# Optimization experiments

Measured on AMD Instinct MI355X. Metric: run time of the kernel, lower is better.

The kernel has to match this reference:

```python
import jax, jax.numpy as jnp
import numpy as np
from jax import lax

THD = 0.8  # Lowe ratio-test threshold (module init kwarg `thd`)


def setup_inputs() -> dict:
    key = jax.random.key(0)
    k1, k2 = jax.random.split(key)
    desc1 = jax.random.normal(k1, (16384, 128), dtype=jnp.float32)
    desc2 = jax.random.normal(k2, (16384, 128), dtype=jnp.float32)
    return {"desc1": desc1, "desc2": desc2}


def _cdist(a, b):
    # Euclidean pairwise distances, (B1, B2), same math as torch.cdist(p=2)
    sq_a = jnp.sum(a * a, axis=-1, keepdims=True)          # (B1, 1)
    sq_b = jnp.sum(b * b, axis=-1)                          # (B2,)
    d2 = sq_a + sq_b - 2.0 * (a @ b.T)                      # (B1, B2)
    return jnp.sqrt(jnp.maximum(d2, 0.0))


def reference(desc1, desc2):
    cost = _cdist(desc1, desc2)                             # (B1, B2)
    # two smallest distances per row
    neg_vals, idxs_in_2 = lax.top_k(-cost, 2)               # (B1, 2) each
    vals = -neg_vals
    ratio = vals[:, 0] / vals[:, 1]                         # (B1,)
    mask = ratio <= THD                                     # (B1,) bool
    # jit-compatible padded outputs: masked-out rows carry 0 distance; the
    # boolean mask selects the valid (idxs_in1, idxs_in2) match rows, which is
    # the compaction torch does with boolean indexing.
    match_dists = jnp.where(mask, ratio, 0.0)               # (B1,)
    idxs_in1 = jnp.arange(desc1.shape[0], dtype=jnp.int32)
    matches_idxs = jnp.stack([idxs_in1, idxs_in_2[:, 0].astype(jnp.int32)], axis=1)  # (B1, 2)
    return match_dists, matches_idxs, mask
```

## Files before the change

kernel.cpp:

```cpp
#include <hip/hip_runtime.h>
#include <math.h>
#include <float.h>
#include <stdint.h>


typedef __attribute__((ext_vector_type(4))) float     f32x4;
typedef __attribute__((ext_vector_type(8))) _Float16  half8;

#define D_     128
#define BM_    256
#define BN_    32
#define CS_    8
#define PARTS_ 8

__device__ __forceinline__ void gload_lds16(const void* g, void* l) {
  auto gp = (const __attribute__((address_space(1))) unsigned int*)(uintptr_t)g;
  auto lp = (__attribute__((address_space(3))) unsigned int*)(uintptr_t)l;
  __builtin_amdgcn_global_load_lds(gp, lp, 16, 0, 0);
}

__global__ void norms_kernel(const float* __restrict__ d1,
                             const float* __restrict__ d2,
                             float* __restrict__ sq, int B) {
  int gid  = blockIdx.x * blockDim.x + threadIdx.x;
  int wid  = gid >> 6;
  int lane = gid & 63;
  if (wid >= 2 * B) return;
  const float* src = (wid < B) ? (d1 + (size_t)wid * D_)
                               : (d2 + (size_t)(wid - B) * D_);
  float2 v = ((const float2*)src)[lane];
  float s = fmaf(v.x, v.x, v.y * v.y);
  #pragma unroll
  for (int off = 32; off > 0; off >>= 1) s += __shfl_down(s, off, 64);
  if (lane == 0) sq[wid] = s;
}

__global__ void convert_kernel(const float* __restrict__ d1, const float* __restrict__ d2,
                               _Float16* __restrict__ Ahi, _Float16* __restrict__ Alo,
                               _Float16* __restrict__ BhiP, _Float16* __restrict__ BloP,
                               int B) {
  int i = blockIdx.x * blockDim.x + threadIdx.x;
  int total = B * 16;
  if (i >= 2 * total) return;
  bool isB = i >= total;
  int j    = isB ? i - total : i;
  int desc = j >> 4;
  int seg  = j & 15;
  const float* src = (isB ? d2 : d1) + (size_t)desc * D_ + seg * 8;
  float4 v0 = *(const float4*)(src);
  float4 v1 = *(const float4*)(src + 4);
  half8 hv, lv;
  float e[8] = {v0.x, v0.y, v0.z, v0.w, v1.x, v1.y, v1.z, v1.w};
  #pragma unroll
  for (int q = 0; q < 8; ++q) {
    _Float16 h = (_Float16)e[q];
    _Float16 l = (_Float16)(e[q] - (float)h);
    if (isB) { h = (_Float16)(-2.0f) * h; l = (_Float16)(-2.0f) * l; }
    hv[q] = h; lv[q] = l;
  }
  if (!isB) {
    *(half8*)(Ahi + (size_t)desc * D_ + seg * 8) = hv;
    *(half8*)(Alo + (size_t)desc * D_ + seg * 8) = lv;
  } else {
    int t   = desc >> 5, cloc = desc & 31;
    int nf  = cloc >> 4, c15  = cloc & 15;
    int kk  = seg >> 2,  gq   = seg & 3;
    size_t off = (size_t)t * 4096 + kk * 1024 + nf * 512 + gq * 128 + c15 * 8;
    *(half8*)(BhiP + off) = hv;
    *(half8*)(BloP + off) = lv;
  }
}

__global__ __launch_bounds__(256, 2)
void nn_mfma(const _Float16* __restrict__ Ahi, const _Float16* __restrict__ Alo,
             const _Float16* __restrict__ BhiP, const _Float16* __restrict__ BloP,
             const float* __restrict__ sqb,
             float* __restrict__ p_d0, float* __restrict__ p_d1,
             int* __restrict__ p_j0, int B) {
  extern __shared__ char smem[];
  float* sq_lds = (float*)(smem + 49152);
  const int tid  = threadIdx.x;
  const int lane = tid & 63;
  const int wid  = tid >> 6;
  const int l15  = lane & 15;
  const int g    = lane >> 4;

  const int nrb   = B / BM_;
  const int rb    = blockIdx.x % nrb;
  const int cspl  = blockIdx.x / nrb;
  const int i0    = rb * BM_;
  const int niter = (B / CS_) / BN_;
  const int tile0 = cspl * niter;

  half8 ah[4][4], al[4][4];
  #pragma unroll
  for (int mf = 0; mf < 4; ++mf) {
    int row = i0 + wid * 64 + mf * 16 + l15;
    const _Float16* pa = Ahi + (size_t)row * D_ + g * 8;
    const _Float16* pl = Alo + (size_t)row * D_ + g * 8;
    #pragma unroll
    for (int kk = 0; kk < 4; ++kk) {
      ah[mf][kk] = *(const half8*)(pa + kk * 32);
      al[mf][kk] = *(const half8*)(pl + kk * 32);
    }
  }

  {
    const float* sqs = sqb + cspl * 2048;
    #pragma unroll
    for (int e = 0; e < 2; ++e) {
      int idx = tid + e * 256;
      float4 v = ((const float4*)sqs)[idx];
      ((float4*)sq_lds)[idx] = v;
    }
  }

  const _Float16* srcW = ((wid < 2) ? BhiP : BloP)
                       + (size_t)tile0 * 4096 + (wid & 1) * 2048 + lane * 8;
  char* ldsW = smem + (wid >> 1) * 8192 + (wid & 1) * 4096;
  auto stage = [&](int bufbase, int it) {
    const _Float16* s = srcW + (size_t)it * 4096;
    char* l = ldsW + bufbase;
    #pragma unroll
    for (int e = 0; e < 4; ++e) gload_lds16(s + e * 512, l + e * 1024);
  };

  float best0[16], best1[16]; int bj[16];
  #pragma unroll
  for (int s = 0; s < 16; ++s) { best0[s] = FLT_MAX; best1[s] = FLT_MAX; bj[s] = 0x7fffffff; }

  const int colg0 = tile0 * BN_ + l15;

  stage(0, 0);
  stage(16384, 1);
  asm volatile("s_waitcnt vmcnt(4)" ::: "memory");
  asm volatile("s_waitcnt lgkmcnt(0)" ::: "memory");
  __builtin_amdgcn_s_barrier();
  asm volatile("" ::: "memory");

  float sjc0 = sq_lds[l15];
  float sjc1 = sq_lds[16 + l15];

  int bcur = 0, bstage = 32768;
  for (int it = 0; it < niter; ++it) {
    if (it + 2 < niter) stage(bstage, it + 2);
    float sjn0 = 0.f, sjn1 = 0.f;
    if (it + 1 < niter) {
      sjn0 = sq_lds[(it + 1) * 32 + l15];
      sjn1 = sq_lds[(it + 1) * 32 + 16 + l15];
    }

    f32x4 acc[4][2];
    __builtin_amdgcn_s_setprio(1);
    #pragma unroll
    for (int kk = 0; kk < 4; ++kk) {
      half8 bh[2], bl[2];
      #pragma unroll
      for (int nf = 0; nf < 2; ++nf) {
        bh[nf] = *(const half8*)(smem + bcur + kk * 2048 + nf * 1024 + lane * 16);
        bl[nf] = *(const half8*)(smem + bcur + 8192 + kk * 2048 + nf * 1024 + lane * 16);
      }
      #pragma unroll
      for (int mf = 0; mf < 4; ++mf)
        #pragma unroll
        for (int nf = 0; nf < 2; ++nf) {
          if (kk == 0) {
            float sj = nf ? sjc1 : sjc0;
            f32x4 c0 = {sj, sj, sj, sj};
            acc[mf][nf] = __builtin_amdgcn_mfma_f32_16x16x32_f16(ah[mf][0], bh[nf], c0, 0, 0, 0);
          } else {
            acc[mf][nf] = __builtin_amdgcn_mfma_f32_16x16x32_f16(ah[mf][kk], bh[nf], acc[mf][nf], 0, 0, 0);
          }
        }
      #pragma unroll
      for (int mf = 0; mf < 4; ++mf)
        #pragma unroll
        for (int nf = 0; nf < 2; ++nf)
          acc[mf][nf] = __builtin_amdgcn_mfma_f32_16x16x32_f16(ah[mf][kk], bl[nf], acc[mf][nf], 0, 0, 0);
      #pragma unroll
      for (int mf = 0; mf < 4; ++mf)
        #pragma unroll
        for (int nf = 0; nf < 2; ++nf)
          acc[mf][nf] = __builtin_amdgcn_mfma_f32_16x16x32_f16(al[mf][kk], bh[nf], acc[mf][nf], 0, 0, 0);
    }
    __builtin_amdgcn_s_setprio(0);

    #pragma unroll
    for (int nf = 0; nf < 2; ++nf) {
      int colg = colg0 + it * BN_ + nf * 16;
      #pragma unroll
      for (int mf = 0; mf < 4; ++mf)
        #pragma unroll
        for (int r = 0; r < 4; ++r) {
          int s = mf * 4 + r;
          float t = acc[mf][nf][r];
          best1[s] = __builtin_amdgcn_fmed3f(t, best0[s], best1[s]);
          bool lt0 = t < best0[s];
          best0[s] = fminf(t, best0[s]);
          bj[s]    = lt0 ? colg : bj[s];
        }
    }

    if (it + 2 < niter) asm volatile("s_waitcnt vmcnt(4)" ::: "memory");
    else                asm volatile("s_waitcnt vmcnt(0)" ::: "memory");
    __builtin_amdgcn_s_barrier();
    asm volatile("" ::: "memory");

    sjc0 = sjn0; sjc1 = sjn1;
    bcur   = (bcur   == 32768) ? 0 : bcur   + 16384;
    bstage = (bstage == 32768) ? 0 : bstage + 16384;
  }

  #pragma unroll
  for (int off = 1; off < 16; off <<= 1) {
    #pragma unroll
    for (int s = 0; s < 16; ++s) {
      float e0 = __shfl_xor(best0[s], off, 64);
      float e1 = __shfl_xor(best1[s], off, 64);
      int   f0 = __shfl_xor(bj[s],    off, 64);
      if (e0 < best0[s] || (e0 == best0[s] && f0 < bj[s])) {
        best1[s] = fminf(best0[s], e1);
        best0[s] = e0;
        bj[s]    = f0;
      } else {
        best1[s] = fminf(best1[s], e0);
      }
    }
  }

  if (l15 == 0) {
    #pragma unroll
    for (int s = 0; s < 16; ++s) {
      int mf = s >> 2, r = s & 3;
      int row = i0 + wid * 64 + mf * 16 + g * 4 + r;
      p_d0[row * PARTS_ + cspl] = best0[s];
      p_d1[row * PARTS_ + cspl] = best1[s];
      p_j0[row * PARTS_ + cspl] = bj[s];
    }
  }
}

__global__ void nn_final(const float* __restrict__ sqa,
                         const float* __restrict__ p_d0,
                         const float* __restrict__ p_d1,
                         const int* __restrict__ p_j0,
                         float* __restrict__ out, int B) {
  int row = blockIdx.x * blockDim.x + threadIdx.x;
  if (row >= B) return;
  float d0 = FLT_MAX, d1 = FLT_MAX;
  int j0 = 0x7fffffff;
  for (int cs = 0; cs < PARTS_; ++cs) {
    float e0 = p_d0[row * PARTS_ + cs];
    float e1 = p_d1[row * PARTS_ + cs];
    int   f0 = p_j0[row * PARTS_ + cs];
    if (e0 < d0 || (e0 == d0 && f0 < j0)) {
      d1 = fminf(d0, e1);
      d0 = e0;
      j0 = f0;
    } else {
      d1 = fminf(d1, e0);
    }
  }
  float sa = sqa[row];
  float v0 = sqrtf(fmaxf(sa + d0, 0.f));
  float v1 = sqrtf(fmaxf(sa + d1, 0.f));
  float ratio = v0 / v1;
  bool m = (ratio <= 0.8f);
  out[row]             = m ? ratio : 0.f;
  out[B + row * 2]     = (float)row;
  out[B + row * 2 + 1] = (float)j0;
  out[3 * B + row]     = m ? 1.f : 0.f;
}

extern "C" void kernel_launch(void* const* d_in, const int* in_sizes, int n_in,
                              void* d_out, int out_size, void* d_ws, size_t ws_size,
                              hipStream_t stream) {
  const float* d1 = (const float*)d_in[0];
  const float* d2 = (const float*)d_in[1];
  const int B = in_sizes[0] / D_;

  float* ws   = (float*)d_ws;
  float* sqa  = ws;
  float* sqb  = ws + B;
  float* p_d0 = ws + 2 * B;
  float* p_d1 = ws + 10 * B;
  int*   p_j0 = (int*)(ws + 18 * B);
  _Float16* Ahi  = (_Float16*)(ws + 26 * B);
  _Float16* Alo  = Ahi + (size_t)B * D_;
  _Float16* BhiP = Alo + (size_t)B * D_;
  _Float16* BloP = BhiP + (size_t)B * D_;

  int nthreads = 2 * B * 64;
  norms_kernel<<<(nthreads + 255) / 256, 256, 0, stream>>>(d1, d2, sqa, B);

  int ngroups = 2 * B * 16;
  convert_kernel<<<(ngroups + 255) / 256, 256, 0, stream>>>(d1, d2, Ahi, Alo, BhiP, BloP, B);

  hipFuncSetAttribute((const void*)nn_mfma,
                      hipFuncAttributeMaxDynamicSharedMemorySize, 57344);
  nn_mfma<<<(B / BM_) * CS_, 256, 57344, stream>>>(Ahi, Alo, BhiP, BloP, sqb,
                                                   p_d0, p_d1, p_j0, B);

  nn_final<<<(B + 255) / 256, 256, 0, stream>>>(sqa, p_d0, p_d1, p_j0, (float*)d_out, B);
}
```

Baseline: 175.4 us.

## Fuse norms into convert kernel and double-buffer B tiles in pairs

Row squared norms are now computed inside the fp16 split conversion kernel with a 16-lane shuffle reduction, which removes the separate norms kernel launch and its second read of the inputs. The main MFMA loop changes from a three-slot ring with one tile per barrier to two slots of two tiles each, so each barrier and wait covers two tiles of compute. This halves the number of barriers but raises LDS to 72 KB per block, which may cost occupancy, and now waits on all outstanding loads (vmcnt(0)) each period.

```diff
diff --git a/kernel.cpp b/kernel.cpp
--- a/kernel.cpp
+++ b/kernel.cpp
@@ -19,26 +19,10 @@
   __builtin_amdgcn_global_load_lds(gp, lp, 16, 0, 0);
 }
 
-__global__ void norms_kernel(const float* __restrict__ d1,
-                             const float* __restrict__ d2,
-                             float* __restrict__ sq, int B) {
-  int gid  = blockIdx.x * blockDim.x + threadIdx.x;
-  int wid  = gid >> 6;
-  int lane = gid & 63;
-  if (wid >= 2 * B) return;
-  const float* src = (wid < B) ? (d1 + (size_t)wid * D_)
-                               : (d2 + (size_t)(wid - B) * D_);
-  float2 v = ((const float2*)src)[lane];
-  float s = fmaf(v.x, v.x, v.y * v.y);
-  #pragma unroll
-  for (int off = 32; off > 0; off >>= 1) s += __shfl_down(s, off, 64);
-  if (lane == 0) sq[wid] = s;
-}
-
 __global__ void convert_kernel(const float* __restrict__ d1, const float* __restrict__ d2,
                                _Float16* __restrict__ Ahi, _Float16* __restrict__ Alo,
                                _Float16* __restrict__ BhiP, _Float16* __restrict__ BloP,
-                               int B) {
+                               float* __restrict__ sq, int B) {
   int i = blockIdx.x * blockDim.x + threadIdx.x;
   int total = B * 16;
   if (i >= 2 * total) return;
@@ -51,13 +35,19 @@
   float4 v1 = *(const float4*)(src + 4);
   half8 hv, lv;
   float e[8] = {v0.x, v0.y, v0.z, v0.w, v1.x, v1.y, v1.z, v1.w};
+  float ss = 0.f;
   #pragma unroll
   for (int q = 0; q < 8; ++q) {
+    ss = fmaf(e[q], e[q], ss);
     _Float16 h = (_Float16)e[q];
     _Float16 l = (_Float16)(e[q] - (float)h);
     if (isB) { h = (_Float16)(-2.0f) * h; l = (_Float16)(-2.0f) * l; }
     hv[q] = h; lv[q] = l;
   }
+  #pragma unroll
+  for (int off = 8; off > 0; off >>= 1) ss += __shfl_xor(ss, off, 64);
+  if (seg == 0) sq[(isB ? B : 0) + desc] = ss;
+
   if (!isB) {
     *(half8*)(Ahi + (size_t)desc * D_ + seg * 8) = hv;
     *(half8*)(Alo + (size_t)desc * D_ + seg * 8) = lv;
@@ -78,7 +68,7 @@
              float* __restrict__ p_d0, float* __restrict__ p_d1,
              int* __restrict__ p_j0, int B) {
   extern __shared__ char smem[];
-  float* sq_lds = (float*)(smem + 49152);
+  float* sq_lds = (float*)(smem + 65536);
   const int tid  = threadIdx.x;
   const int lane = tid & 63;
   const int wid  = tid >> 6;
@@ -89,8 +79,8 @@
   const int rb    = blockIdx.x % nrb;
   const int cspl  = blockIdx.x / nrb;
   const int i0    = rb * BM_;
-  const int niter = (B / CS_) / BN_;
-  const int tile0 = cspl * niter;
+  const int ntile = (B / CS_) / BN_;
+  const int tile0 = cspl * ntile;
 
   half8 ah[4][4], al[4][4];
   #pragma unroll
@@ -118,9 +108,9 @@
   const _Float16* srcW = ((wid < 2) ? BhiP : BloP)
                        + (size_t)tile0 * 4096 + (wid & 1) * 2048 + lane * 8;
   char* ldsW = smem + (wid >> 1) * 8192 + (wid & 1) * 4096;
-  auto stage = [&](int bufbase, int it) {
-    const _Float16* s = srcW + (size_t)it * 4096;
-    char* l = ldsW + bufbase;
+  auto stage = [&](int slotbase, int t) {
+    const _Float16* s = srcW + (size_t)t * 4096;
+    char* l = ldsW + slotbase;
     #pragma unroll
     for (int e = 0; e < 4; ++e) gload_lds16(s + e * 512, l + e * 1024);
   };
@@ -131,25 +121,9 @@
 
   const int colg0 = tile0 * BN_ + l15;
 
-  stage(0, 0);
-  stage(16384, 1);
-  asm volatile("s_waitcnt vmcnt(4)" ::: "memory");
-  asm volatile("s_waitcnt lgkmcnt(0)" ::: "memory");
-  __builtin_amdgcn_s_barrier();
-  asm volatile("" ::: "memory");
-
-  float sjc0 = sq_lds[l15];
-  float sjc1 = sq_lds[16 + l15];
-
-  int bcur = 0, bstage = 32768;
-  for (int it = 0; it < niter; ++it) {
-    if (it + 2 < niter) stage(bstage, it + 2);
-    float sjn0 = 0.f, sjn1 = 0.f;
-    if (it + 1 < niter) {
-      sjn0 = sq_lds[(it + 1) * 32 + l15];
-      sjn1 = sq_lds[(it + 1) * 32 + 16 + l15];
-    }
-
+  auto tilecomp = [&](int t, int sb) {
+    float sjc0 = sq_lds[t * 32 + l15];
+    float sjc1 = sq_lds[t * 32 + 16 + l15];
     f32x4 acc[4][2];
     __builtin_amdgcn_s_setprio(1);
     #pragma unroll
@@ -157,8 +131,8 @@
       half8 bh[2], bl[2];
       #pragma unroll
       for (int nf = 0; nf < 2; ++nf) {
-        bh[nf] = *(const half8*)(smem + bcur + kk * 2048 + nf * 1024 + lane * 16);
-        bl[nf] = *(const half8*)(smem + bcur + 8192 + kk * 2048 + nf * 1024 + lane * 16);
+        bh[nf] = *(const half8*)(smem + sb + kk * 2048 + nf * 1024 + lane * 16);
+        bl[nf] = *(const half8*)(smem + sb + 8192 + kk * 2048 + nf * 1024 + lane * 16);
       }
       #pragma unroll
       for (int mf = 0; mf < 4; ++mf)
@@ -187,28 +161,42 @@
 
     #pragma unroll
     for (int nf = 0; nf < 2; ++nf) {
-      int colg = colg0 + it * BN_ + nf * 16;
+      int colg = colg0 + t * BN_ + nf * 16;
       #pragma unroll
       for (int mf = 0; mf < 4; ++mf)
         #pragma unroll
         for (int r = 0; r < 4; ++r) {
           int s = mf * 4 + r;
-          float t = acc[mf][nf][r];
-          best1[s] = __builtin_amdgcn_fmed3f(t, best0[s], best1[s]);
-          bool lt0 = t < best0[s];
-          best0[s] = fminf(t, best0[s]);
+          float v = acc[mf][nf][r];
+          best1[s] = __builtin_amdgcn_fmed3f(v, best0[s], best1[s]);
+          bool lt0 = v < best0[s];
+          best0[s] = fminf(v, best0[s]);
           bj[s]    = lt0 ? colg : bj[s];
         }
     }
-
-    if (it + 2 < niter) asm volatile("s_waitcnt vmcnt(4)" ::: "memory");
-    else                asm volatile("s_waitcnt vmcnt(0)" ::: "memory");
+  };
+
+  stage(0, 0);
+  stage(16384, 1);
+  asm volatile("s_waitcnt vmcnt(0)" ::: "memory");
+  asm volatile("s_waitcnt lgkmcnt(0)" ::: "memory");
+  __builtin_amdgcn_s_barrier();
+  asm volatile("" ::: "memory");
+
+  const int nper = ntile / 2;
+  for (int p = 0; p < nper; ++p) {
+    const int sbcur = (p & 1) * 32768;
+    if (p + 1 < nper) {
+      stage(sbcur ^ 32768, 2 * p + 2);
+      stage((sbcur ^ 32768) + 16384, 2 * p + 3);
+    }
+
+    tilecomp(2 * p,     sbcur);
+    tilecomp(2 * p + 1, sbcur + 16384);
+
+    asm volatile("s_waitcnt vmcnt(0)" ::: "memory");
     __builtin_amdgcn_s_barrier();
     asm volatile("" ::: "memory");
-
-    sjc0 = sjn0; sjc1 = sjn1;
-    bcur   = (bcur   == 32768) ? 0 : bcur   + 16384;
-    bstage = (bstage == 32768) ? 0 : bstage + 16384;
   }
 
   #pragma unroll
@@ -290,15 +278,12 @@
   _Float16* BhiP = Alo + (size_t)B * D_;
   _Float16* BloP = BhiP + (size_t)B * D_;
 
-  int nthreads = 2 * B * 64;
-  norms_kernel<<<(nthreads + 255) / 256, 256, 0, stream>>>(d1, d2, sqa, B);
-
   int ngroups = 2 * B * 16;
-  convert_kernel<<<(ngroups + 255) / 256, 256, 0, stream>>>(d1, d2, Ahi, Alo, BhiP, BloP, B);
+  convert_kernel<<<(ngroups + 255) / 256, 256, 0, stream>>>(d1, d2, Ahi, Alo, BhiP, BloP, sqa, B);
 
   hipFuncSetAttribute((const void*)nn_mfma,
-                      hipFuncAttributeMaxDynamicSharedMemorySize, 57344);
-  nn_mfma<<<(B / BM_) * CS_, 256, 57344, stream>>>(Ahi, Alo, BhiP, BloP, sqb,
+                      hipFuncAttributeMaxDynamicSharedMemorySize, 73728);
+  nn_mfma<<<(B / BM_) * CS_, 256, 73728, stream>>>(Ahi, Alo, BhiP, BloP, sqb,
                                                    p_d0, p_d1, p_j0, B);
 
   nn_final<<<(B + 255) / 256, 256, 0, stream>>>(sqa, p_d0, p_d1, p_j0, (float*)d_out, B);
```

Measured after the change: 173.9 us. No clear change (-0.9%).
